# Performance work log

Hardware: AMD Instinct MI355X
Metric: run time of the kernel (lower is better)

The kernel has to match this reference:

```python
import jax, jax.numpy as jnp
import numpy as np

E = 2048   # embedding_size
H = 16     # n_heads
D = E // H # head_dimension = 128
B = 4
N = 2048


def setup_inputs() -> dict:
    key = jax.random.key(0)
    ks = jax.random.split(key, 5)
    scale_qkv = 1.0 / np.sqrt(E)
    scale_fc = 1.0 / np.sqrt(E)
    return {
        "x": jax.random.normal(ks[0], (B, N, E), dtype=jnp.float32),
        # torch Linear(E, E + 2*D); stored as [in, out] for x @ W
        "w_qkv": jax.random.uniform(ks[1], (E, E + 2 * D), jnp.float32, -scale_qkv, scale_qkv),
        "b_qkv": jax.random.uniform(ks[2], (E + 2 * D,), jnp.float32, -scale_qkv, scale_qkv),
        "w_fc": jax.random.uniform(ks[3], (E, E), jnp.float32, -scale_fc, scale_fc),
        "b_fc": jax.random.uniform(ks[4], (E,), jnp.float32, -scale_fc, scale_fc),
    }


def reference(x, w_qkv, b_qkv, w_fc, b_fc):
    b, n, _ = x.shape
    qkv = x @ w_qkv + b_qkv                         # [B,N,E+2D]
    q = qkv[..., :E].reshape(b, n, H, D)            # [B,N,H,D]
    k = qkv[..., E:E + D]                           # [B,N,D] single KV head (MQA)
    v = qkv[..., E + D:]                            # [B,N,D]
    # scores: queries per head against shared keys
    scores = jnp.einsum("bnhd,bmd->bhnm", q, k) / jnp.sqrt(jnp.float32(D))
    # causal mask: triu(ones, diagonal=1) positions filled with -inf
    causal = jnp.triu(jnp.ones((n, n), dtype=bool), k=1)
    scores = jnp.where(causal, -jnp.inf, scores)
    attn = jax.nn.softmax(scores, axis=-1)          # [B,H,N,N]
    out = jnp.einsum("bhnm,bmd->bnhd", attn, v)     # [B,N,H,D]
    out = out.reshape(b, n, E)
    return out @ w_fc + b_fc                        # dropout=0 (eval): identity
```

## Files before the change

kernel.cpp:

```cpp
#include <hip/hip_runtime.h>

#define E_DIM 2048
#define H_NUM 16
#define D_HEAD 128
#define B_SZ 4
#define N_SEQ 2048
#define QKV_LD 2304
#define MROWS_T (B_SZ * N_SEQ)
#define PLS 40
#define SC2F 0.12751744802582937f

typedef __attribute__((ext_vector_type(8))) __bf16 bfx8;
typedef __attribute__((ext_vector_type(8))) short sx8;
typedef __attribute__((ext_vector_type(4))) short sx4;
typedef __attribute__((ext_vector_type(2))) short sx2;
typedef __attribute__((ext_vector_type(4))) float fx4;

__device__ __forceinline__ fx4 mfma_bf16(bfx8 a, bfx8 b, fx4 c) {
    return __builtin_amdgcn_mfma_f32_16x16x32_bf16(a, b, c, 0, 0, 0);
}

__device__ __forceinline__ short f2bf(float f) {
    unsigned u = __builtin_bit_cast(unsigned, f);
    u += 0x7FFFu + ((u >> 16) & 1u);
    return (short)(u >> 16);
}

__device__ __forceinline__ int cvt_pk_bf16(float a, float b) {
    int r;
    asm("v_cvt_pk_bf16_f32 %0, %1, %2" : "=v"(r) : "v"(a), "v"(b));
    return r;
}

__device__ __forceinline__ void gld_lds16(const void* g, void* l) {
    __builtin_amdgcn_global_load_lds((__attribute__((address_space(1))) void*)(void*)g,
                                     (__attribute__((address_space(3))) void*)l, 16, 0, 0);
}

__global__ __launch_bounds__(256) void cast_f32_bf16(const float* __restrict__ in,
                                                     short* __restrict__ out, int n) {
    int i = (blockIdx.x * 256 + threadIdx.x) * 4;
    if (i >= n) return;
    float4 v = *(const float4*)(in + i);
    sx4 r = {f2bf(v.x), f2bf(v.y), f2bf(v.z), f2bf(v.w)};
    *(sx4*)(out + i) = r;
}

__global__ __launch_bounds__(256) void transpose_cast(const float* __restrict__ in,
                                                      short* __restrict__ out, int R, int C) {
    __shared__ float tile[32][33];
    int c0 = blockIdx.x * 32, r0 = blockIdx.y * 32;
    int tx = threadIdx.x;
    for (int i = threadIdx.y; i < 32; i += 8)
        tile[i][tx] = in[(size_t)(r0 + i) * C + c0 + tx];
    __syncthreads();
    for (int i = threadIdx.y; i < 32; i += 8)
        out[(size_t)(c0 + i) * R + r0 + tx] = f2bf(tile[tx][i]);
}

__global__ __launch_bounds__(256) void v_transpose(const short* __restrict__ qkv,
                                                   short* __restrict__ vtg) {
    __shared__ short tile[32][33];
    int r0 = blockIdx.x * 32;
    int d0 = blockIdx.y * 32;
    int tx = threadIdx.x;
    for (int i = threadIdx.y; i < 32; i += 8)
        tile[i][tx] = qkv[(size_t)(r0 + i) * QKV_LD + (E_DIM + D_HEAD) + d0 + tx];
    __syncthreads();
    int kp = ((tx & 15) << 1) | (tx >> 4);
    for (int i = threadIdx.y; i < 32; i += 8)
        vtg[(size_t)(d0 + i) * MROWS_T + r0 + kp] = tile[tx][i];
}

template <bool OUT_BF16, bool SCALE_Q>
__global__ __launch_bounds__(256) void gemm_bt(const short* __restrict__ A,
                                               const short* __restrict__ Bt,
                                               const float* __restrict__ bias,
                                               void* __restrict__ Cp,
                                               int M, int N, int K) {
    __shared__ __align__(16) short As[128 * 32];
    __shared__ __align__(16) short Bs[128 * 32];
    const int tid = threadIdx.x, wave = tid >> 6, lane = tid & 63;
    const int quad = lane >> 4, l16 = lane & 15;

    const int gx = gridDim.x;
    int wg = blockIdx.y * gx + blockIdx.x;
    {
        const int nwg = gx * gridDim.y;
        const int qd = nwg >> 3, rm = nwg & 7;
        const int xcd = wg & 7, loc = wg >> 3;
        wg = (xcd < rm ? xcd * (qd + 1) : rm * (qd + 1) + (xcd - rm) * qd) + loc;
    }
    const int m0 = (wg / gx) * 128, n0 = (wg % gx) * 128;

    const int wm = (wave >> 1) * 64, wn = (wave & 1) * 64;
    const int srow = lane >> 2, scol = (lane & 3) * 8;

    fx4 acc[4][4];
#pragma unroll
    for (int mt = 0; mt < 4; ++mt)
#pragma unroll
        for (int nt = 0; nt < 4; ++nt) acc[mt][nt] = (fx4){0.f, 0.f, 0.f, 0.f};

    const short* Ag = A + (size_t)m0 * K;
    const short* Bg = Bt + (size_t)n0 * K;

    for (int k0 = 0; k0 < K; k0 += 32) {
#pragma unroll
        for (int i = 0; i < 2; ++i) {
            int chunk = wave * 2 + i;
            int row = chunk * 16 + srow;
            gld_lds16(Ag + (size_t)row * K + k0 + scol, &As[chunk * 512]);
            gld_lds16(Bg + (size_t)row * K + k0 + scol, &Bs[chunk * 512]);
        }
        __syncthreads();
        bfx8 af[4], bfr[4];
#pragma unroll
        for (int t = 0; t < 4; ++t) {
            af[t]  = *(const bfx8*)&As[(wm + t * 16 + l16) * 32 + quad * 8];
            bfr[t] = *(const bfx8*)&Bs[(wn + t * 16 + l16) * 32 + quad * 8];
        }
#pragma unroll
        for (int mt = 0; mt < 4; ++mt)
#pragma unroll
            for (int nt = 0; nt < 4; ++nt)
                acc[mt][nt] = mfma_bf16(af[mt], bfr[nt], acc[mt][nt]);
        __syncthreads();
    }

    const float scl = (SCALE_Q && n0 < E_DIM) ? SC2F : 1.0f;
    float bv[4];
#pragma unroll
    for (int nt = 0; nt < 4; ++nt) bv[nt] = bias[n0 + wn + nt * 16 + l16];

#pragma unroll
    for (int mt = 0; mt < 4; ++mt)
#pragma unroll
        for (int nt = 0; nt < 4; ++nt)
#pragma unroll
            for (int j = 0; j < 4; ++j) {
                int row = m0 + wm + mt * 16 + quad * 4 + j;
                int col = n0 + wn + nt * 16 + l16;
                float v = (acc[mt][nt][j] + bv[nt]) * scl;
                if (OUT_BF16)
                    ((short*)Cp)[(size_t)row * N + col] = f2bf(v);
                else
                    ((float*)Cp)[(size_t)row * N + col] = v;
            }
}

__global__ __launch_bounds__(256, 2) void attn_kernel(const short* __restrict__ qkv,
                                                      const short* __restrict__ vtg,
                                                      short* __restrict__ outp) {
    __shared__ __align__(16) short Ks[2][4096];
    __shared__ __align__(16) short Vt[2][4096];
    __shared__ __align__(16) short pl[4 * 32 * PLS];
    const int b = blockIdx.y >> 4, h = blockIdx.y & 15;
    const int tid = threadIdx.x, wave = tid >> 6, lane = tid & 63;
    const int quad = lane >> 4, l16 = lane & 15;
    const int srow = lane >> 2, sq = lane & 3;
    const size_t baseRow = (size_t)b * N_SEQ;
    short* plw = pl + wave * 32 * PLS;

    auto stage = [&](int k0, int bufi) {
#pragma unroll
        for (int i = 0; i < 2; ++i) {
            const int c = wave * 2 + i;
            gld_lds16(qkv + (baseRow + k0 + (c & 1) * 16 + srow) * QKV_LD + E_DIM +
                          (c >> 1) * 32 + sq * 8,
                      &Ks[bufi][c * 512]);
            gld_lds16(vtg + (size_t)(c * 16 + srow) * MROWS_T + baseRow + k0 + sq * 8,
                      &Vt[bufi][c * 512]);
        }
    };

#pragma unroll 1
    for (int half = 0; half < 2; ++half) {
        const int chunk = half ? (15 - blockIdx.x) : blockIdx.x;
        const int q0 = chunk * 128;
        const int wrow = q0 + wave * 32;

        bfx8 aq0[4], aq1[4];
        {
            const short* qb0 = qkv + (baseRow + wrow + l16) * QKV_LD + h * D_HEAD + quad * 8;
            const short* qb1 = qb0 + 16 * QKV_LD;
#pragma unroll
            for (int c = 0; c < 4; ++c) {
                aq0[c] = *(const bfx8*)(qb0 + c * 32);
                aq1[c] = *(const bfx8*)(qb1 + c * 32);
            }
        }

        fx4 accO0[8], accO1[8];
        float l0[4], l1[4];
#pragma unroll
        for (int dt = 0; dt < 8; ++dt) {
            accO0[dt] = (fx4){0.f, 0.f, 0.f, 0.f};
            accO1[dt] = (fx4){0.f, 0.f, 0.f, 0.f};
        }
#pragma unroll
        for (int j = 0; j < 4; ++j) { l0[j] = 0.f; l1[j] = 0.f; }

        const int nbulk = 4 * chunk;
        const int nkt = nbulk + 4;

        __syncthreads();
        stage(0, 0);

#pragma unroll 1
        for (int kt = 0; kt < nkt; ++kt) {
            __syncthreads();
            if (kt + 1 < nkt) stage((kt + 1) << 5, (kt + 1) & 1);
            const short* ks = Ks[kt & 1];
            const short* vs = Vt[kt & 1];
            const int k0 = kt << 5;

            fx4 s00 = {0.f, 0.f, 0.f, 0.f}, s01 = {0.f, 0.f, 0.f, 0.f};
            fx4 s10 = {0.f, 0.f, 0.f, 0.f}, s11 = {0.f, 0.f, 0.f, 0.f};
            __builtin_amdgcn_s_setprio(1);
#pragma unroll
            for (int dc = 0; dc < 4; ++dc) {
                bfx8 kf0 = *(const bfx8*)&ks[(dc * 2 + 0) * 512 + l16 * 32 + quad * 8];
                bfx8 kf1 = *(const bfx8*)&ks[(dc * 2 + 1) * 512 + l16 * 32 + quad * 8];
                s00 = mfma_bf16(aq0[dc], kf0, s00);
                s01 = mfma_bf16(aq0[dc], kf1, s01);
                s10 = mfma_bf16(aq1[dc], kf0, s10);
                s11 = mfma_bf16(aq1[dc], kf1, s11);
            }
            __builtin_amdgcn_s_setprio(0);

            const bool diag = kt >= nbulk;
#pragma unroll
            for (int j = 0; j < 4; ++j) {
                float e0 = __builtin_amdgcn_exp2f(s00[j]);
                float e1 = __builtin_amdgcn_exp2f(s01[j]);
                if (diag) {
                    const int rb = wrow + quad * 4 + j;
                    e0 = (k0 + l16 <= rb) ? e0 : 0.f;
                    e1 = (k0 + 16 + l16 <= rb) ? e1 : 0.f;
                }
                l0[j] += e0 + e1;
                int pk = cvt_pk_bf16(e0, e1);
                *(sx2*)&plw[(quad * 4 + j) * PLS + 2 * l16] = __builtin_bit_cast(sx2, pk);
            }
#pragma unroll
            for (int j = 0; j < 4; ++j) {
                float e0 = __builtin_amdgcn_exp2f(s10[j]);
                float e1 = __builtin_amdgcn_exp2f(s11[j]);
                if (diag) {
                    const int rb = wrow + 16 + quad * 4 + j;
                    e0 = (k0 + l16 <= rb) ? e0 : 0.f;
                    e1 = (k0 + 16 + l16 <= rb) ? e1 : 0.f;
                }
                l1[j] += e0 + e1;
                int pk = cvt_pk_bf16(e0, e1);
                *(sx2*)&plw[(16 + quad * 4 + j) * PLS + 2 * l16] = __builtin_bit_cast(sx2, pk);
            }

            sx8 aps0 = *(const sx8*)&plw[l16 * PLS + quad * 8];
            sx8 aps1 = *(const sx8*)&plw[(16 + l16) * PLS + quad * 8];
            bfx8 ap0 = __builtin_bit_cast(bfx8, aps0);
            bfx8 ap1 = __builtin_bit_cast(bfx8, aps1);
            __builtin_amdgcn_s_setprio(1);
#pragma unroll
            for (int dt = 0; dt < 8; ++dt) {
                bfx8 bv = *(const bfx8*)&vs[dt * 512 + l16 * 32 + quad * 8];
                accO0[dt] = mfma_bf16(ap0, bv, accO0[dt]);
                accO1[dt] = mfma_bf16(ap1, bv, accO1[dt]);
            }
            __builtin_amdgcn_s_setprio(0);
        }

#pragma unroll
        for (int off = 1; off < 16; off <<= 1)
#pragma unroll
            for (int j = 0; j < 4; ++j) {
                l0[j] += __shfl_xor(l0[j], off);
                l1[j] += __shfl_xor(l1[j], off);
            }
#pragma unroll
        for (int j = 0; j < 4; ++j) {
            float rl0 = 1.0f / l0[j];
            float rl1 = 1.0f / l1[j];
            size_t ob0 = (baseRow + wrow + quad * 4 + j) * (size_t)E_DIM + h * D_HEAD + l16;
            size_t ob1 = ob0 + (size_t)16 * E_DIM;
#pragma unroll
            for (int dt = 0; dt < 8; ++dt) {
                outp[ob0 + dt * 16] = f2bf(accO0[dt][j] * rl0);
                outp[ob1 + dt * 16] = f2bf(accO1[dt][j] * rl1);
            }
        }
    }
}

extern "C" void kernel_launch(void* const* d_in, const int* in_sizes, int n_in,
                              void* d_out, int out_size, void* d_ws, size_t ws_size,
                              hipStream_t stream) {
    const float* x     = (const float*)d_in[0];
    const float* w_qkv = (const float*)d_in[1];
    const float* b_qkv = (const float*)d_in[2];
    const float* w_fc  = (const float*)d_in[3];
    const float* b_fc  = (const float*)d_in[4];
    float* out = (float*)d_out;

    const size_t MROWS = (size_t)B_SZ * N_SEQ;
    short* xb    = (short*)d_ws;
    short* wqkvt = xb + MROWS * E_DIM;
    short* wfct  = wqkvt + (size_t)QKV_LD * E_DIM;
    short* qkvb  = wfct + (size_t)E_DIM * E_DIM;
    short* attnb = qkvb + MROWS * QKV_LD;
    short* vtg   = xb;

    cast_f32_bf16<<<dim3((int)(MROWS * E_DIM / 1024)), dim3(256), 0, stream>>>(
        x, xb, (int)(MROWS * E_DIM));
    transpose_cast<<<dim3(QKV_LD / 32, E_DIM / 32), dim3(32, 8), 0, stream>>>(
        w_qkv, wqkvt, E_DIM, QKV_LD);
    transpose_cast<<<dim3(E_DIM / 32, E_DIM / 32), dim3(32, 8), 0, stream>>>(
        w_fc, wfct, E_DIM, E_DIM);

    gemm_bt<true, true><<<dim3(QKV_LD / 128, (int)(MROWS / 128)), dim3(256), 0, stream>>>(
        xb, wqkvt, b_qkv, qkvb, (int)MROWS, QKV_LD, E_DIM);

    v_transpose<<<dim3(MROWS_T / 32, D_HEAD / 32), dim3(32, 8), 0, stream>>>(qkvb, vtg);

    attn_kernel<<<dim3(8, B_SZ * H_NUM), dim3(256), 0, stream>>>(qkvb, vtg, attnb);

    gemm_bt<false, false><<<dim3(E_DIM / 128, (int)(MROWS / 128)), dim3(256), 0, stream>>>(
        attnb, wfct, b_fc, out, (int)MROWS, E_DIM, E_DIM);
}
```

Before: 466.1 us.

## Add 256x256-tile pipelined GEMM kernel for QKV and output projections

```diff
diff --git a/kernel.cpp b/kernel.cpp
--- a/kernel.cpp
+++ b/kernel.cpp
@@ -77,7 +77,7 @@
                                                const short* __restrict__ Bt,
                                                const float* __restrict__ bias,
                                                void* __restrict__ Cp,
-                                               int M, int N, int K) {
+                                               int M, int N, int ldc, int K) {
     __shared__ __align__(16) short As[128 * 32];
     __shared__ __align__(16) short Bs[128 * 32];
     const int tid = threadIdx.x, wave = tid >> 6, lane = tid & 63;
@@ -143,9 +143,148 @@
                 int col = n0 + wn + nt * 16 + l16;
                 float v = (acc[mt][nt][j] + bv[nt]) * scl;
                 if (OUT_BF16)
-                    ((short*)Cp)[(size_t)row * N + col] = f2bf(v);
+                    ((short*)Cp)[(size_t)row * ldc + col] = f2bf(v);
                 else
-                    ((float*)Cp)[(size_t)row * N + col] = v;
+                    ((float*)Cp)[(size_t)row * ldc + col] = v;
+            }
+}
+
+template <bool OUT_BF16, bool SCALE_ALL>
+__global__ __launch_bounds__(512) void gemm256(const short* __restrict__ A,
+                                               const short* __restrict__ Bt,
+                                               const float* __restrict__ bias,
+                                               void* __restrict__ Cp,
+                                               int M, int N, int ldc, int K) {
+    __shared__ __align__(16) short lds[2][2][2][8192];
+    const int tid = threadIdx.x, wave = tid >> 6, lane = tid & 63;
+    const int quad = lane >> 4, l16 = lane & 15;
+    const int wmi = wave >> 2, wni = wave & 3;
+    const int m0 = blockIdx.y * 256, n0 = blockIdx.x * 256;
+
+    const size_t rstep = (size_t)128 * K;
+    const int srow = wave * 16 + (lane >> 2);
+    const int sslot = (lane & 3) ^ ((lane >> 3) & 3);
+    const short* Asrc = A + ((size_t)(m0 + srow)) * K + sslot * 8;
+    const short* Bsrc = Bt + ((size_t)(n0 + srow)) * K + sslot * 8;
+
+    auto stage = [&](const short* srcb, short* dstb, int kcol0) {
+        gld_lds16(srcb + kcol0, dstb + wave * 512);
+        gld_lds16(srcb + kcol0 + rstep, dstb + 4096 + wave * 512);
+    };
+
+    const int swl = (l16 >> 1) & 3;
+    const int aoff = (wmi * 128 + l16) * 32 + (quad ^ swl) * 8;
+    const int boff = (wni * 64 + l16) * 32 + (quad ^ swl) * 8;
+
+    fx4 acc[8][4];
+#pragma unroll
+    for (int m = 0; m < 8; ++m)
+#pragma unroll
+        for (int n = 0; n < 4; ++n) acc[m][n] = (fx4){0.f, 0.f, 0.f, 0.f};
+
+    const int nt = K >> 6;
+
+    stage(Asrc, &lds[0][0][0][0], 0);
+    stage(Bsrc, &lds[0][0][1][0], 0);
+    stage(Asrc, &lds[0][1][0][0], 32);
+    stage(Bsrc, &lds[0][1][1][0], 32);
+    stage(Asrc, &lds[1][0][0][0], 64);
+    stage(Bsrc, &lds[1][0][1][0], 64);
+    asm volatile("s_waitcnt vmcnt(4)");
+    __builtin_amdgcn_s_barrier();
+    __builtin_amdgcn_sched_barrier(0);
+
+#pragma unroll 1
+    for (int t = 0; t < nt; ++t) {
+        const int cur = t & 1, nxt = cur ^ 1;
+        const short* Ah0 = &lds[cur][0][0][0];
+        const short* Bh0 = &lds[cur][0][1][0];
+        const short* Ah1 = &lds[cur][1][0][0];
+        const short* Bh1 = &lds[cur][1][1][0];
+        const int kc = t * 64;
+        bfx8 af[4], bf0[4], bf1[4];
+
+#pragma unroll
+        for (int n = 0; n < 4; ++n) bf0[n] = *(const bfx8*)&Bh0[boff + n * 512];
+#pragma unroll
+        for (int m = 0; m < 4; ++m) af[m] = *(const bfx8*)&Ah0[aoff + m * 512];
+        if (t + 1 < nt) stage(Asrc, &lds[nxt][1][0][0], kc + 96);
+        __builtin_amdgcn_s_barrier();
+        __builtin_amdgcn_sched_barrier(0);
+        __builtin_amdgcn_s_setprio(1);
+#pragma unroll
+        for (int m = 0; m < 4; ++m)
+#pragma unroll
+            for (int n = 0; n < 4; ++n) acc[m][n] = mfma_bf16(af[m], bf0[n], acc[m][n]);
+        __builtin_amdgcn_s_setprio(0);
+        __builtin_amdgcn_s_barrier();
+        __builtin_amdgcn_sched_barrier(0);
+
+#pragma unroll
+        for (int m = 0; m < 4; ++m) af[m] = *(const bfx8*)&Ah0[aoff + (m + 4) * 512];
+        if (t + 1 < nt) stage(Bsrc, &lds[nxt][1][1][0], kc + 96);
+        __builtin_amdgcn_s_barrier();
+        __builtin_amdgcn_sched_barrier(0);
+        __builtin_amdgcn_s_setprio(1);
+#pragma unroll
+        for (int m = 0; m < 4; ++m)
+#pragma unroll
+            for (int n = 0; n < 4; ++n) acc[m + 4][n] = mfma_bf16(af[m], bf0[n], acc[m + 4][n]);
+        __builtin_amdgcn_s_setprio(0);
+        __builtin_amdgcn_s_barrier();
+        __builtin_amdgcn_sched_barrier(0);
+
+#pragma unroll
+        for (int n = 0; n < 4; ++n) bf1[n] = *(const bfx8*)&Bh1[boff + n * 512];
+#pragma unroll
+        for (int m = 0; m < 4; ++m) af[m] = *(const bfx8*)&Ah1[aoff + m * 512];
+        if (t + 2 < nt) stage(Asrc, &lds[cur][0][0][0], kc + 128);
+        __builtin_amdgcn_s_barrier();
+        __builtin_amdgcn_sched_barrier(0);
+        __builtin_amdgcn_s_setprio(1);
+#pragma unroll
+        for (int m = 0; m < 4; ++m)
+#pragma unroll
+            for (int n = 0; n < 4; ++n) acc[m][n] = mfma_bf16(af[m], bf1[n], acc[m][n]);
+        __builtin_amdgcn_s_setprio(0);
+        __builtin_amdgcn_s_barrier();
+        __builtin_amdgcn_sched_barrier(0);
+
+#pragma unroll
+        for (int m = 0; m < 4; ++m) af[m] = *(const bfx8*)&Ah1[aoff + (m + 4) * 512];
+        if (t + 2 < nt) stage(Bsrc, &lds[cur][0][1][0], kc + 128);
+        __builtin_amdgcn_s_barrier();
+        __builtin_amdgcn_sched_barrier(0);
+        __builtin_amdgcn_s_setprio(1);
+#pragma unroll
+        for (int m = 0; m < 4; ++m)
+#pragma unroll
+            for (int n = 0; n < 4; ++n) acc[m + 4][n] = mfma_bf16(af[m], bf1[n], acc[m + 4][n]);
+        __builtin_amdgcn_s_setprio(0);
+        if (t < nt - 2) asm volatile("s_waitcnt vmcnt(4)");
+        else            asm volatile("s_waitcnt vmcnt(0)");
+        __builtin_amdgcn_s_barrier();
+        __builtin_amdgcn_sched_barrier(0);
+    }
+
+    const float scl = SCALE_ALL ? SC2F : 1.0f;
+    float bvn[4];
+#pragma unroll
+    for (int n = 0; n < 4; ++n) bvn[n] = bias[n0 + wni * 64 + n * 16 + l16];
+
+#pragma unroll
+    for (int m = 0; m < 8; ++m)
+#pragma unroll
+        for (int n = 0; n < 4; ++n)
+#pragma unroll
+            for (int j = 0; j < 4; ++j) {
+                int row = m0 + wmi * 128 + m * 16 + quad * 4 + j;
+                int col = n0 + wni * 64 + n * 16 + l16;
+                float v = (acc[m][n][j] + bvn[n]) * scl;
+                if (OUT_BF16)
+                    ((short*)Cp)[(size_t)row * ldc + col] = f2bf(v);
+                else
+                    ((float*)Cp)[(size_t)row * ldc + col] = v;
             }
 }
 
@@ -318,13 +457,16 @@
     transpose_cast<<<dim3(E_DIM / 32, E_DIM / 32), dim3(32, 8), 0, stream>>>(
         w_fc, wfct, E_DIM, E_DIM);
 
-    gemm_bt<true, true><<<dim3(QKV_LD / 128, (int)(MROWS / 128)), dim3(256), 0, stream>>>(
-        xb, wqkvt, b_qkv, qkvb, (int)MROWS, QKV_LD, E_DIM);
+    gemm256<true, true><<<dim3(E_DIM / 256, (int)(MROWS / 256)), dim3(512), 0, stream>>>(
+        xb, wqkvt, b_qkv, qkvb, (int)MROWS, E_DIM, QKV_LD, E_DIM);
+    gemm_bt<true, false><<<dim3(2, (int)(MROWS / 128)), dim3(256), 0, stream>>>(
+        xb, wqkvt + (size_t)E_DIM * E_DIM, b_qkv + E_DIM, qkvb + E_DIM,
+        (int)MROWS, 2 * D_HEAD, QKV_LD, E_DIM);
 
     v_transpose<<<dim3(MROWS_T / 32, D_HEAD / 32), dim3(32, 8), 0, stream>>>(qkvb, vtg);
 
     attn_kernel<<<dim3(8, B_SZ * H_NUM), dim3(256), 0, stream>>>(qkvb, vtg, attnb);
 
-    gemm_bt<false, false><<<dim3(E_DIM / 128, (int)(MROWS / 128)), dim3(256), 0, stream>>>(
-        attnb, wfct, b_fc, out, (int)MROWS, E_DIM, E_DIM);
-}
+    gemm256<false, false><<<dim3(E_DIM / 256, (int)(MROWS / 256)), dim3(512), 0, stream>>>(
+        attnb, wfct, b_fc, out, (int)MROWS, E_DIM, E_DIM, E_DIM);
+}
```

Result: faster. 438.1 us (-6.0%).
